# Kernel tuning notes

Measured on AMD Instinct MI355X. Metric: run time of the kernel, lower is better.

## Reference

```python
import jax, jax.numpy as jnp
import numpy as np

N = 100_000      # nodes
F_IN = 512       # input feature dim
HID = 8          # hidden per head (layer 1)
HEADS = 8        # heads layer 1
CLS = 7          # num classes (layer 2 out, 1 head)
E = 1_600_000    # random edges (self-loops added in reference)
NEG_SLOPE = 0.2  # PyG GATConv default leaky_relu slope


def setup_inputs() -> dict:
    key = jax.random.key(0)
    ks = jax.random.split(key, 10)
    s1 = 1.0 / np.sqrt(F_IN)
    s2 = 1.0 / np.sqrt(HID * HEADS)
    return {
        "x": jax.random.normal(ks[0], (N, F_IN), jnp.float32),
        "edge_index": jax.random.randint(ks[1], (2, E), 0, N, dtype=jnp.int32),
        "W1": jax.random.normal(ks[2], (F_IN, HEADS * HID), jnp.float32) * s1,
        "a_src1": jax.random.normal(ks[3], (HEADS, HID), jnp.float32) * s1,
        "a_dst1": jax.random.normal(ks[4], (HEADS, HID), jnp.float32) * s1,
        "b1": jnp.zeros((HEADS * HID,), jnp.float32),
        "W2": jax.random.normal(ks[5], (HEADS * HID, CLS), jnp.float32) * s2,
        "a_src2": jax.random.normal(ks[6], (1, CLS), jnp.float32) * s2,
        "a_dst2": jax.random.normal(ks[7], (1, CLS), jnp.float32) * s2,
        "b2": jnp.zeros((CLS,), jnp.float32),
    }


def gat_layer(x, edge_index, W, a_src, a_dst, bias, concat):
    """PyG GATConv (eval mode): linear -> per-edge LeakyReLU score -> edge-softmax over
    incoming edges per dst node -> weighted scatter-sum of src messages."""
    n = x.shape[0]
    H, C = a_src.shape
    h = (x @ W).reshape(n, H, C)                      # [N, H, C]
    src, dst = edge_index[0], edge_index[1]
    alpha_src = (h * a_src).sum(-1)                   # [N, H]
    alpha_dst = (h * a_dst).sum(-1)                   # [N, H]
    e = jax.nn.leaky_relu(alpha_src[src] + alpha_dst[dst], NEG_SLOPE)  # [E, H]
    # numerically stable segment softmax over edges grouped by dst
    m = jax.ops.segment_max(e, dst, num_segments=n)   # [N, H]
    p = jnp.exp(e - m[dst])                           # [E, H]
    denom = jax.ops.segment_sum(p, dst, num_segments=n)
    alpha = p / denom[dst]                            # [E, H]
    out = jax.ops.segment_sum(alpha[:, :, None] * h[src], dst, num_segments=n)  # [N, H, C]
    out = out.reshape(n, H * C) if concat else out.mean(axis=1)
    return out + bias


def reference(x, edge_index, W1, a_src1, a_dst1, b1, W2, a_src2, a_dst2, b2):
    # add self-loops (GATConv default add_self_loops=True)
    loops = jnp.arange(N, dtype=edge_index.dtype)
    ei = jnp.concatenate([edge_index, jnp.stack([loops, loops])], axis=1)
    h = jax.nn.elu(gat_layer(x, ei, W1, a_src1, a_dst1, b1, concat=True))
    out = gat_layer(h, ei, W2, a_src2, a_dst2, b2, concat=False)
    return jax.nn.log_softmax(out, axis=1)
```

## Files before the change

kernel.cpp:

```cpp
#include <hip/hip_runtime.h>
#include <hip/hip_bf16.h>

#define NEG_SLOPE 0.2f
#define GB 256
#define HWG 384

typedef __attribute__((ext_vector_type(8))) short bfrag;
typedef __attribute__((ext_vector_type(4))) float f32x4;
typedef unsigned short ushort_t;

__device__ __forceinline__ float lrelu(float x) {
    return x >= 0.0f ? x : NEG_SLOPE * x;
}
__device__ __forceinline__ unsigned short f2bf(float f) {
    unsigned int u = __float_as_uint(f);
    u += 0x7fffu + ((u >> 16) & 1u);
    return (unsigned short)(u >> 16);
}
__device__ __forceinline__ float bf2f(unsigned short h) {
    return __uint_as_float(((unsigned int)h) << 16);
}
__device__ __forceinline__ float u2lo(unsigned int u) {
    return __uint_as_float(u << 16);
}
__device__ __forceinline__ float u2hi(unsigned int u) {
    return __uint_as_float(u & 0xffff0000u);
}

__global__ __launch_bounds__(256) void hist_prep_kernel(
    const int* __restrict__ edst, int* __restrict__ bcnt, int E, int NB,
    const float* __restrict__ W1, ushort_t* __restrict__ Whi,
    ushort_t* __restrict__ Wlo) {
    if (blockIdx.x < 128) {
        int t = blockIdx.x * 256 + threadIdx.x;
        int k = t >> 6, c = t & 63;
        float w = W1[t];
        unsigned short hi = f2bf(w);
        float rem = w - bf2f(hi);
        int dst = (k >> 7) * 8192 + c * 128 + (k & 127);
        Whi[dst] = hi;
        Wlo[dst] = f2bf(rem);
        return;
    }
    __shared__ int hist[512];
    int tid = threadIdx.x;
    for (int i = tid; i < NB; i += 256) hist[i] = 0;
    __syncthreads();
    int wg = blockIdx.x - 128;
    int CH = (E + HWG - 1) / HWG;
    int st = wg * CH, en = min(st + CH, E);
    for (int i = st + tid; i < en; i += 256)
        atomicAdd(&hist[edst[i] >> 8], 1);
    __syncthreads();
    for (int i = tid; i < NB; i += 256)
        if (hist[i] > 0) atomicAdd(&bcnt[i], hist[i]);
}

__global__ __launch_bounds__(512) void bscan_kernel(
    const int* __restrict__ bcnt, int* __restrict__ boff, int* __restrict__ bcur,
    int* __restrict__ csr_off, int NB, int N, int E) {
    __shared__ int s[512];
    int t = threadIdx.x;
    int v = (t < NB) ? bcnt[t] : 0;
    s[t] = v;
    __syncthreads();
    for (int off = 1; off < 512; off <<= 1) {
        int tv = (t >= off) ? s[t - off] : 0;
        __syncthreads();
        s[t] += tv;
        __syncthreads();
    }
    if (t < NB) {
        int o = s[t] - v;
        boff[t] = o;
        bcur[t] = o;
    }
    if (t == 0) {
        boff[NB] = E;
        csr_off[N] = E;
    }
}

__global__ __launch_bounds__(1024, 4) void gemm_bscatter_kernel(
    const float* __restrict__ x, const ushort_t* __restrict__ Whi,
    const ushort_t* __restrict__ Wlo, ushort_t* __restrict__ h1b, int n,
    const int* __restrict__ esrc, const int* __restrict__ edst,
    int* __restrict__ bcur, int2* __restrict__ ebuf, int E, int NB,
    const float* __restrict__ a_src1, const float* __restrict__ a_dst1,
    float* __restrict__ as1, float* __restrict__ ad1) {
    __shared__ __align__(16) ushort_t Wh[32768];
    __shared__ __align__(16) ushort_t Wl[32768];
    const int tid = threadIdx.x;

    {
        int* hist = (int*)Wh;
        int* base = hist + 512;
        int* rank = hist + 1024;
        for (int i = tid; i < NB; i += 1024) { hist[i] = 0; rank[i] = 0; }
        __syncthreads();
        int CH = (E + GB - 1) / GB;
        int st = blockIdx.x * CH, en = min(st + CH, E);
        for (int i = st + tid; i < en; i += 1024)
            atomicAdd(&hist[edst[i] >> 8], 1);
        __syncthreads();
        for (int b = tid; b < NB; b += 1024)
            if (hist[b] > 0) base[b] = atomicAdd(&bcur[b], hist[b]);
        __syncthreads();
        for (int i = st + tid; i < en; i += 1024) {
            int d = edst[i], s = esrc[i];
            int b = d >> 8;
            int r = atomicAdd(&rank[b], 1);
            ebuf[base[b] + r] = make_int2(s, d);
        }
        __syncthreads();
    }

    #pragma unroll
    for (int i = 0; i < 4; i++) {
        int lin = (tid + i * 1024) * 8;
        int row = (lin >> 7) & 63;
        int swz = lin ^ ((row & 7) << 3);
        *(bfrag*)&Wh[swz] = *(const bfrag*)&Whi[lin];
        *(bfrag*)&Wl[swz] = *(const bfrag*)&Wlo[lin];
    }
    __syncthreads();

    const int lane = tid & 63;
    const int wave = tid >> 6;
    const int l15 = lane & 15;
    const int lq = lane >> 4;
    const int r7s = (l15 & 7) << 3;

    const int ntiles = (n + 15) >> 4;
    const int tstride = GB * 16;

    for (int tile = blockIdx.x * 16 + wave; tile < ntiles; tile += tstride) {
        const int wb = tile * 16;
        f32x4 acc[4];
        #pragma unroll
        for (int t = 0; t < 4; t++) acc[t] = (f32x4){0.f, 0.f, 0.f, 0.f};

        const int arow = min(wb + l15, n - 1);
        const float* xr = x + (size_t)arow * 512;

        #pragma unroll 1
        for (int p = 0; p < 4; p++) {
            #pragma unroll
            for (int step = 0; step < 4; step++) {
                int kloc = step * 32 + lq * 8;
                int kb = p * 128 + kloc;
                float4 v0 = *(const float4*)&xr[kb];
                float4 v1 = *(const float4*)&xr[kb + 4];
                float xf[8] = {v0.x, v0.y, v0.z, v0.w, v1.x, v1.y, v1.z, v1.w};
                bfrag ah, al;
                #pragma unroll
                for (int j = 0; j < 8; j++) {
                    unsigned short hi = f2bf(xf[j]);
                    float rem = xf[j] - bf2f(hi);
                    ah[j] = (short)hi;
                    al[j] = (short)f2bf(rem);
                }
                #pragma unroll
                for (int t = 0; t < 4; t++) {
                    int nrow = t * 16 + l15;
                    int bidx = ((p * 64 + nrow) * 128 + kloc) ^ r7s;
                    bfrag bh = *(const bfrag*)&Wh[bidx];
                    bfrag bl = *(const bfrag*)&Wl[bidx];
                    acc[t] = __builtin_amdgcn_mfma_f32_16x16x32_bf16(al, bh, acc[t], 0, 0, 0);
                    acc[t] = __builtin_amdgcn_mfma_f32_16x16x32_bf16(ah, bl, acc[t], 0, 0, 0);
                    acc[t] = __builtin_amdgcn_mfma_f32_16x16x32_bf16(ah, bh, acc[t], 0, 0, 0);
                }
            }
        }
        #pragma unroll
        for (int t = 0; t < 4; t++) {
            #pragma unroll
            for (int reg = 0; reg < 4; reg++) {
                int grow = wb + lq * 4 + reg;
                if (grow < n) h1b[(size_t)grow * 64 + t * 16 + l15] = f2bf(acc[t][reg]);
            }
        }
        const int j7 = l15 & 7;
        const int wrow = wb + lq * 4 + (j7 & 3);
        #pragma unroll
        for (int t = 0; t < 4; t++) {
            int cidx = t * 16 + l15;
            float cs = a_src1[cidx];
            float cd = a_dst1[cidx];
            float ps0 = acc[t][0] * cs, ps1 = acc[t][1] * cs;
            float ps2 = acc[t][2] * cs, ps3 = acc[t][3] * cs;
            float pd0 = acc[t][0] * cd, pd1 = acc[t][1] * cd;
            float pd2 = acc[t][2] * cd, pd3 = acc[t][3] * cd;
            #pragma unroll
            for (int off = 1; off < 8; off <<= 1) {
                ps0 += __shfl_xor(ps0, off);
                ps1 += __shfl_xor(ps1, off);
                ps2 += __shfl_xor(ps2, off);
                ps3 += __shfl_xor(ps3, off);
                pd0 += __shfl_xor(pd0, off);
                pd1 += __shfl_xor(pd1, off);
                pd2 += __shfl_xor(pd2, off);
                pd3 += __shfl_xor(pd3, off);
            }
            int h = (t << 1) | (l15 >> 3);
            if (wrow < n) {
                if (j7 < 4) {
                    float sv = j7 == 0 ? ps0 : j7 == 1 ? ps1 : j7 == 2 ? ps2 : ps3;
                    as1[wrow * 8 + h] = sv;
                } else {
                    float dv = j7 == 4 ? pd0 : j7 == 5 ? pd1 : j7 == 6 ? pd2 : pd3;
                    ad1[wrow * 8 + h] = dv;
                }
            }
        }
    }
}

__global__ __launch_bounds__(256) void finalize_kernel(
    const int* __restrict__ boff, const int2* __restrict__ ebuf,
    int* __restrict__ csr_off, int* __restrict__ col, int N, int NB) {
    int tid = threadIdx.x;
    int b = blockIdx.x;
    __shared__ int cnt[256];
    __shared__ int cur[256];
    __shared__ int sc[256];
    cnt[tid] = 0;
    __syncthreads();
    int st = boff[b], en = boff[b + 1];
    for (int i = st + tid; i < en; i += 256)
        atomicAdd(&cnt[ebuf[i].y & 255], 1);
    __syncthreads();
    int v = cnt[tid];
    sc[tid] = v;
    __syncthreads();
    for (int off = 1; off < 256; off <<= 1) {
        int tv = (tid >= off) ? sc[tid - off] : 0;
        __syncthreads();
        sc[tid] += tv;
        __syncthreads();
    }
    int dbase = b << 8;
    int nd = min(256, N - dbase);
    int o = st + sc[tid] - v;
    if (tid < nd) {
        csr_off[dbase + tid] = o;
        cur[tid] = o;
    }
    __syncthreads();
    for (int i = st + tid; i < en; i += 256) {
        int2 p = ebuf[i];
        int r = atomicAdd(&cur[p.y & 255], 1);
        col[r] = p.x;
    }
}

__global__ __launch_bounds__(256) void agg1_kernel(
    const int* __restrict__ csr_off, const int* __restrict__ col,
    const ushort_t* __restrict__ h1b, const float* __restrict__ as1,
    const float* __restrict__ ad1,
    const float* __restrict__ b1, const float* __restrict__ W2,
    const float* __restrict__ a_src2, const float* __restrict__ a_dst2,
    float* __restrict__ g2, float* __restrict__ ad2, int n) {
    int d = blockIdx.x * 8 + (threadIdx.x >> 5);
    if (d >= n) return;
    int c = threadIdx.x & 31;
    int hd = c >> 2;
    const ushort_t* myrow = h1b + (size_t)d * 64;
    float adh = ad1[d * 8 + hd];
    float asd = as1[d * 8 + hd];
    float p0 = __expf(lrelu(asd + adh));
    unsigned int u = *(const unsigned int*)(myrow + c * 2);
    float denom = p0;
    float acc0 = p0 * u2lo(u);
    float acc1 = p0 * u2hi(u);
    int st = csr_off[d], en = csr_off[d + 1];
    int e = st;
    for (; e + 4 <= en; e += 4) {
        int s0 = col[e], s1 = col[e + 1], s2 = col[e + 2], s3 = col[e + 3];
        const ushort_t* r0 = h1b + (size_t)s0 * 64;
        const ushort_t* r1 = h1b + (size_t)s1 * 64;
        const ushort_t* r2 = h1b + (size_t)s2 * 64;
        const ushort_t* r3 = h1b + (size_t)s3 * 64;
        float a0 = as1[s0 * 8 + hd];
        float a1 = as1[s1 * 8 + hd];
        float a2 = as1[s2 * 8 + hd];
        float a3 = as1[s3 * 8 + hd];
        unsigned int u0 = *(const unsigned int*)(r0 + c * 2);
        unsigned int u1 = *(const unsigned int*)(r1 + c * 2);
        unsigned int u2 = *(const unsigned int*)(r2 + c * 2);
        unsigned int u3 = *(const unsigned int*)(r3 + c * 2);
        float q0 = __expf(lrelu(a0 + adh));
        float q1 = __expf(lrelu(a1 + adh));
        float q2 = __expf(lrelu(a2 + adh));
        float q3 = __expf(lrelu(a3 + adh));
        denom += (q0 + q1) + (q2 + q3);
        acc0 = fmaf(q0, u2lo(u0), acc0);
        acc1 = fmaf(q0, u2hi(u0), acc1);
        acc0 = fmaf(q1, u2lo(u1), acc0);
        acc1 = fmaf(q1, u2hi(u1), acc1);
        acc0 = fmaf(q2, u2lo(u2), acc0);
        acc1 = fmaf(q2, u2hi(u2), acc1);
        acc0 = fmaf(q3, u2lo(u3), acc0);
        acc1 = fmaf(q3, u2hi(u3), acc1);
    }
    for (; e < en; ++e) {
        int s0 = col[e];
        const ushort_t* r0 = h1b + (size_t)s0 * 64;
        float a0 = as1[s0 * 8 + hd];
        unsigned int u0 = *(const unsigned int*)(r0 + c * 2);
        float q0 = __expf(lrelu(a0 + adh));
        denom += q0;
        acc0 = fmaf(q0, u2lo(u0), acc0);
        acc1 = fmaf(q0, u2hi(u0), acc1);
    }
    float v0 = acc0 / denom + b1[2 * c];
    float v1 = acc1 / denom + b1[2 * c + 1];
    float h0 = v0 > 0.f ? v0 : (__expf(v0) - 1.f);
    float h1v = v1 > 0.f ? v1 : (__expf(v1) - 1.f);
    float g[7];
    #pragma unroll
    for (int j = 0; j < 7; j++) {
        float t = fmaf(h0, W2[(2 * c) * 7 + j], h1v * W2[(2 * c + 1) * 7 + j]);
        #pragma unroll
        for (int off = 1; off < 32; off <<= 1) t += __shfl_xor(t, off);
        g[j] = t;
    }
    float sa = 0.f, da = 0.f;
    #pragma unroll
    for (int j = 0; j < 7; j++) {
        sa = fmaf(g[j], a_src2[j], sa);
        da = fmaf(g[j], a_dst2[j], da);
    }
    if (c < 7) g2[(size_t)d * 8 + c] = g[c];
    if (c == 7) g2[(size_t)d * 8 + 7] = sa;
    if (c == 8) ad2[d] = da;
}

__global__ __launch_bounds__(256) void agg2_kernel(
    const int* __restrict__ csr_off, const int* __restrict__ col,
    const float* __restrict__ ad2, const float* __restrict__ g2,
    const float* __restrict__ b2, float* __restrict__ out, int n) {
    int d = blockIdx.x * 4 + (threadIdx.x >> 6);
    if (d >= n) return;
    int lane = threadIdx.x & 63;
    int j = lane >> 3, cc = lane & 7;
    int bl = lane | 7;
    float adv = ad2[d];
    float vd = g2[(size_t)d * 8 + cc];
    float as2d = __shfl(vd, bl);
    float pd = (j == 0) ? __expf(lrelu(as2d + adv)) : 0.f;
    float denom = pd;
    float acc = pd * vd;
    int st = csr_off[d], en = csr_off[d + 1];
    for (int base = st; base < en; base += 8) {
        int eidx = base + j;
        bool valid = eidx < en;
        int s = valid ? col[eidx] : d;
        float val = g2[(size_t)s * 8 + cc];
        float as2s = __shfl(val, bl);
        float p = valid ? __expf(lrelu(as2s + adv)) : 0.f;
        denom += p;
        acc = fmaf(p, val, acc);
    }
    #pragma unroll
    for (int off = 8; off < 64; off <<= 1) {
        acc += __shfl_xor(acc, off);
        denom += __shfl_xor(denom, off);
    }
    float o = acc / denom + ((cc < 7) ? b2[cc] : 0.f);
    float m = (cc < 7) ? o : -1e30f;
    #pragma unroll
    for (int off = 1; off < 8; off <<= 1) m = fmaxf(m, __shfl_xor(m, off));
    float se = (cc < 7) ? __expf(o - m) : 0.f;
    #pragma unroll
    for (int off = 1; off < 8; off <<= 1) se += __shfl_xor(se, off);
    float lse = m + __logf(se);
    if (j == 0 && cc < 7) out[(size_t)d * 7 + cc] = o - lse;
}

extern "C" void kernel_launch(void* const* d_in, const int* in_sizes, int n_in,
                              void* d_out, int out_size, void* d_ws, size_t ws_size,
                              hipStream_t stream) {
    const float* x      = (const float*)d_in[0];
    const int*   ei     = (const int*)d_in[1];
    const float* W1     = (const float*)d_in[2];
    const float* a_src1 = (const float*)d_in[3];
    const float* a_dst1 = (const float*)d_in[4];
    const float* b1     = (const float*)d_in[5];
    const float* W2     = (const float*)d_in[6];
    const float* a_src2 = (const float*)d_in[7];
    const float* a_dst2 = (const float*)d_in[8];
    const float* b2     = (const float*)d_in[9];

    int N = in_sizes[0] / 512;
    int E = in_sizes[1] / 2;
    const int* esrc = ei;
    const int* edst = ei + E;
    int NB = (N + 255) >> 8;

    char* ws = (char*)d_ws;
    size_t off = 0;
    auto alloc = [&](size_t bytes) -> void* {
        void* p = ws + off;
        off += (bytes + 255) & ~(size_t)255;
        return p;
    };
    ushort_t* h1b  = (ushort_t*)alloc((size_t)N * 64 * 2);
    float* as1     = (float*)alloc((size_t)N * 8 * 4);
    float* ad1     = (float*)alloc((size_t)N * 8 * 4);
    float* g2      = (float*)alloc((size_t)N * 8 * 4);
    float* ad2     = (float*)alloc((size_t)N * 4);
    int*   csr_off = (int*)alloc((size_t)(N + 1) * 4);
    int*   col     = (int*)alloc((size_t)E * 4);
    int2*  ebuf    = (int2*)alloc((size_t)E * 8);
    ushort_t* Whi  = (ushort_t*)alloc(512 * 64 * 2);
    ushort_t* Wlo  = (ushort_t*)alloc(512 * 64 * 2);
    int*   bcnt    = (int*)alloc((size_t)NB * 4);
    int*   boff    = (int*)alloc((size_t)(NB + 1) * 4);
    int*   bcur    = (int*)alloc((size_t)NB * 4);

    hipMemsetAsync(bcnt, 0, (size_t)NB * 4, stream);

    hist_prep_kernel<<<128 + HWG, 256, 0, stream>>>(edst, bcnt, E, NB, W1, Whi, Wlo);
    bscan_kernel<<<1, 512, 0, stream>>>(bcnt, boff, bcur, csr_off, NB, N, E);
    gemm_bscatter_kernel<<<GB, 1024, 0, stream>>>(x, Whi, Wlo, h1b, N,
                                                  esrc, edst, bcur, ebuf, E, NB,
                                                  a_src1, a_dst1, as1, ad1);
    finalize_kernel<<<NB, 256, 0, stream>>>(boff, ebuf, csr_off, col, N, NB);
    agg1_kernel<<<(N + 7) / 8, 256, 0, stream>>>(csr_off, col, h1b, as1, ad1, b1,
                                                 W2, a_src2, a_dst2, g2, ad2, N);
    agg2_kernel<<<(N + 3) / 4, 256, 0, stream>>>(csr_off, col, ad2, g2, b2,
                                                 (float*)d_out, N);
}
```

Measured before the change: 467.4 us.

## Split edge bucket scatter from GEMM and use deterministic 2D count scan

Moves the edge bucketing scatter out of the GEMM kernel into its own kernel. The per-chunk histograms become a 2D count table, and a column scan over it replaces the global atomic bucket cursor and the per-block recount of edges. Each edge record is packed into one int (src<<8 | dst low byte) instead of an int2, which halves ebuf traffic. The cost is two extra kernel launches. The GEMM no longer overlaps the scatter inside the same blocks, and the packing assumes src fits in 24 bits.

```diff
diff --git a/kernel.cpp b/kernel.cpp
--- a/kernel.cpp
+++ b/kernel.cpp
@@ -2,8 +2,7 @@
 #include <hip/hip_bf16.h>
 
 #define NEG_SLOPE 0.2f
-#define GB 256
-#define HWG 384
+#define SBK 256
 
 typedef __attribute__((ext_vector_type(8))) short bfrag;
 typedef __attribute__((ext_vector_type(4))) float f32x4;
@@ -28,7 +27,7 @@
 }
 
 __global__ __launch_bounds__(256) void hist_prep_kernel(
-    const int* __restrict__ edst, int* __restrict__ bcnt, int E, int NB,
+    const int* __restrict__ edst, int* __restrict__ cnt2d, int E, int NB,
     const float* __restrict__ W1, ushort_t* __restrict__ Whi,
     ushort_t* __restrict__ Wlo) {
     if (blockIdx.x < 128) {
@@ -44,20 +43,38 @@
     }
     __shared__ int hist[512];
     int tid = threadIdx.x;
-    for (int i = tid; i < NB; i += 256) hist[i] = 0;
-    __syncthreads();
-    int wg = blockIdx.x - 128;
-    int CH = (E + HWG - 1) / HWG;
-    int st = wg * CH, en = min(st + CH, E);
+    for (int i = tid; i < 512; i += 256) hist[i] = 0;
+    __syncthreads();
+    int s = blockIdx.x - 128;
+    int CH = (E + SBK - 1) / SBK;
+    int st = s * CH, en = min(st + CH, E);
     for (int i = st + tid; i < en; i += 256)
         atomicAdd(&hist[edst[i] >> 8], 1);
     __syncthreads();
-    for (int i = tid; i < NB; i += 256)
-        if (hist[i] > 0) atomicAdd(&bcnt[i], hist[i]);
+    for (int b = tid; b < NB; b += 256)
+        cnt2d[b * SBK + s] = hist[b];
+}
+
+__global__ __launch_bounds__(256) void scan_cols_kernel(
+    int* __restrict__ cnt2d, int* __restrict__ bcnt, int NB) {
+    int b = blockIdx.x;
+    int t = threadIdx.x;
+    __shared__ int sc[256];
+    int v = cnt2d[b * SBK + t];
+    sc[t] = v;
+    __syncthreads();
+    for (int off = 1; off < 256; off <<= 1) {
+        int tv = (t >= off) ? sc[t - off] : 0;
+        __syncthreads();
+        sc[t] += tv;
+        __syncthreads();
+    }
+    cnt2d[b * SBK + t] = sc[t] - v;
+    if (t == 255) bcnt[b] = sc[255];
 }
 
 __global__ __launch_bounds__(512) void bscan_kernel(
-    const int* __restrict__ bcnt, int* __restrict__ boff, int* __restrict__ bcur,
+    const int* __restrict__ bcnt, int* __restrict__ boff,
     int* __restrict__ csr_off, int NB, int N, int E) {
     __shared__ int s[512];
     int t = threadIdx.x;
@@ -70,50 +87,44 @@
         s[t] += tv;
         __syncthreads();
     }
-    if (t < NB) {
-        int o = s[t] - v;
-        boff[t] = o;
-        bcur[t] = o;
-    }
+    if (t < NB) boff[t] = s[t] - v;
     if (t == 0) {
         boff[NB] = E;
         csr_off[N] = E;
     }
 }
 
-__global__ __launch_bounds__(1024, 4) void gemm_bscatter_kernel(
+__global__ __launch_bounds__(1024) void scatter_kernel(
+    const int* __restrict__ esrc, const int* __restrict__ edst,
+    const int* __restrict__ boff, const int* __restrict__ cnt2d,
+    int* __restrict__ ebuf, int E, int NB) {
+    __shared__ int base[512];
+    __shared__ int rank[512];
+    int tid = threadIdx.x;
+    int s = blockIdx.x;
+    for (int b = tid; b < NB; b += 1024) {
+        base[b] = boff[b] + cnt2d[b * SBK + s];
+        rank[b] = 0;
+    }
+    __syncthreads();
+    int CH = (E + SBK - 1) / SBK;
+    int st = s * CH, en = min(st + CH, E);
+    for (int i = st + tid; i < en; i += 1024) {
+        int d = edst[i];
+        int b = d >> 8;
+        int r = atomicAdd(&rank[b], 1);
+        ebuf[base[b] + r] = (esrc[i] << 8) | (d & 255);
+    }
+}
+
+__global__ __launch_bounds__(1024, 4) void gemm_kernel(
     const float* __restrict__ x, const ushort_t* __restrict__ Whi,
     const ushort_t* __restrict__ Wlo, ushort_t* __restrict__ h1b, int n,
-    const int* __restrict__ esrc, const int* __restrict__ edst,
-    int* __restrict__ bcur, int2* __restrict__ ebuf, int E, int NB,
     const float* __restrict__ a_src1, const float* __restrict__ a_dst1,
     float* __restrict__ as1, float* __restrict__ ad1) {
     __shared__ __align__(16) ushort_t Wh[32768];
     __shared__ __align__(16) ushort_t Wl[32768];
     const int tid = threadIdx.x;
-
-    {
-        int* hist = (int*)Wh;
-        int* base = hist + 512;
-        int* rank = hist + 1024;
-        for (int i = tid; i < NB; i += 1024) { hist[i] = 0; rank[i] = 0; }
-        __syncthreads();
-        int CH = (E + GB - 1) / GB;
-        int st = blockIdx.x * CH, en = min(st + CH, E);
-        for (int i = st + tid; i < en; i += 1024)
-            atomicAdd(&hist[edst[i] >> 8], 1);
-        __syncthreads();
-        for (int b = tid; b < NB; b += 1024)
-            if (hist[b] > 0) base[b] = atomicAdd(&bcur[b], hist[b]);
-        __syncthreads();
-        for (int i = st + tid; i < en; i += 1024) {
-            int d = edst[i], s = esrc[i];
-            int b = d >> 8;
-            int r = atomicAdd(&rank[b], 1);
-            ebuf[base[b] + r] = make_int2(s, d);
-        }
-        __syncthreads();
-    }
 
     #pragma unroll
     for (int i = 0; i < 4; i++) {
@@ -132,7 +143,7 @@
     const int r7s = (l15 & 7) << 3;
 
     const int ntiles = (n + 15) >> 4;
-    const int tstride = GB * 16;
+    const int tstride = 256 * 16;
 
     for (int tile = blockIdx.x * 16 + wave; tile < ntiles; tile += tstride) {
         const int wb = tile * 16;
@@ -217,7 +228,7 @@
 }
 
 __global__ __launch_bounds__(256) void finalize_kernel(
-    const int* __restrict__ boff, const int2* __restrict__ ebuf,
+    const int* __restrict__ boff, const int* __restrict__ ebuf,
     int* __restrict__ csr_off, int* __restrict__ col, int N, int NB) {
     int tid = threadIdx.x;
     int b = blockIdx.x;
@@ -228,7 +239,7 @@
     __syncthreads();
     int st = boff[b], en = boff[b + 1];
     for (int i = st + tid; i < en; i += 256)
-        atomicAdd(&cnt[ebuf[i].y & 255], 1);
+        atomicAdd(&cnt[ebuf[i] & 255], 1);
     __syncthreads();
     int v = cnt[tid];
     sc[tid] = v;
@@ -248,9 +259,9 @@
     }
     __syncthreads();
     for (int i = st + tid; i < en; i += 256) {
-        int2 p = ebuf[i];
-        int r = atomicAdd(&cur[p.y & 255], 1);
-        col[r] = p.x;
+        int p = ebuf[i];
+        int r = atomicAdd(&cur[p & 255], 1);
+        col[r] = ((unsigned int)p) >> 8;
     }
 }
 
@@ -412,20 +423,19 @@
     float* ad2     = (float*)alloc((size_t)N * 4);
     int*   csr_off = (int*)alloc((size_t)(N + 1) * 4);
     int*   col     = (int*)alloc((size_t)E * 4);
-    int2*  ebuf    = (int2*)alloc((size_t)E * 8);
+    int*   ebuf    = (int*)alloc((size_t)E * 4);
     ushort_t* Whi  = (ushort_t*)alloc(512 * 64 * 2);
     ushort_t* Wlo  = (ushort_t*)alloc(512 * 64 * 2);
+    int*   cnt2d   = (int*)alloc((size_t)NB * SBK * 4);
     int*   bcnt    = (int*)alloc((size_t)NB * 4);
     int*   boff    = (int*)alloc((size_t)(NB + 1) * 4);
-    int*   bcur    = (int*)alloc((size_t)NB * 4);
-
-    hipMemsetAsync(bcnt, 0, (size_t)NB * 4, stream);
-
-    hist_prep_kernel<<<128 + HWG, 256, 0, stream>>>(edst, bcnt, E, NB, W1, Whi, Wlo);
-    bscan_kernel<<<1, 512, 0, stream>>>(bcnt, boff, bcur, csr_off, NB, N, E);
-    gemm_bscatter_kernel<<<GB, 1024, 0, stream>>>(x, Whi, Wlo, h1b, N,
-                                                  esrc, edst, bcur, ebuf, E, NB,
-                                                  a_src1, a_dst1, as1, ad1);
+
+    hist_prep_kernel<<<128 + SBK, 256, 0, stream>>>(edst, cnt2d, E, NB, W1, Whi, Wlo);
+    scan_cols_kernel<<<NB, 256, 0, stream>>>(cnt2d, bcnt, NB);
+    bscan_kernel<<<1, 512, 0, stream>>>(bcnt, boff, csr_off, NB, N, E);
+    scatter_kernel<<<SBK, 1024, 0, stream>>>(esrc, edst, boff, cnt2d, ebuf, E, NB);
+    gemm_kernel<<<256, 1024, 0, stream>>>(x, Whi, Wlo, h1b, N,
+                                          a_src1, a_dst1, as1, ad1);
     finalize_kernel<<<NB, 256, 0, stream>>>(boff, ebuf, csr_off, col, N, NB);
     agg1_kernel<<<(N + 7) / 8, 256, 0, stream>>>(csr_off, col, h1b, as1, ad1, b1,
                                                  W2, a_src2, a_dst2, g2, ad2, N);
```

Result: no change. 463.7 us (-0.8%).
